# Kernel tuning notes

Hardware: AMD Instinct MI355X
Metric: run time of the kernel (lower is better)

Reference implementation:

```python
import jax, jax.numpy as jnp
import numpy as np

B_, L, HID = 2, 1024, 2048
N, H, P, NA = 128, 64, 64, 32   # state, heads, head_dim, rope angle pairs
DIN = 2 * H * P + 2 * N + 3 * H + NA  # 8672
EPS = 1e-5
A_FLOOR = 1e-4


def setup_inputs() -> dict:
    key = jax.random.key(0)
    k0, k1, k2 = jax.random.split(key, 3)
    hidden_states = jax.random.normal(k0, (B_, L, HID), jnp.float32)
    in_proj_w = jax.random.normal(k1, (DIN, HID), jnp.float32) * 0.02
    out_proj_w = jax.random.normal(k2, (HID, H * P), jnp.float32) * 0.02
    # dt_bias init exactly as in the torch module
    rng = np.random.default_rng(0)
    dt = np.exp(rng.random(H) * (np.log(0.1) - np.log(0.001)) + np.log(0.001))
    dt = np.clip(dt, 1e-4, None)
    dt_bias = jnp.asarray(dt + np.log(-np.expm1(-dt)), jnp.float32)
    return {
        'hidden_states': hidden_states,
        'in_proj_w': in_proj_w,
        'dt_bias': dt_bias,
        'B_bias': jnp.ones((H, N), jnp.float32),
        'C_bias': jnp.ones((H, N), jnp.float32),
        'B_norm_w': jnp.ones((N,), jnp.float32),
        'C_norm_w': jnp.ones((N,), jnp.float32),
        'D': jnp.ones((H,), jnp.float32),
        'out_proj_w': out_proj_w,
    }


def _rmsnorm(x, w):
    var = jnp.mean(jnp.square(x), axis=-1, keepdims=True)
    return x * jax.lax.rsqrt(var + EPS) * w


def _forward(hidden_states, in_proj_w, dt_bias, B_bias, C_bias,
             B_norm_w, C_norm_w, D, out_proj_w):
    b, l, _ = hidden_states.shape
    proj = hidden_states @ in_proj_w.T  # (b,l,DIN)
    splits = np.cumsum([H * P, H * P, N, N, H, H, H])
    z, x, Braw, Craw, dd_dt, dd_A, trap, angles = jnp.split(proj, splits, axis=-1)
    z = z.reshape(b, l, H, P)
    x = x.reshape(b, l, H, P)
    # data-dependent A (per token, per head), clamped
    A = jnp.minimum(-jax.nn.softplus(dd_A.astype(jnp.float32)), -A_FLOOR)
    DT = jax.nn.softplus(dd_dt + dt_bias)          # (b,l,H)
    decay = jnp.exp(A * DT)                        # (b,l,H)
    lam = jax.nn.sigmoid(trap)                     # trapezoidal weight (b,l,H)
    # RMSNorm then per-head input-independent bias (n_groups=1, mimo_rank=1)
    Bn = _rmsnorm(Braw, B_norm_w)[:, :, None, :] + B_bias  # (b,l,H,N)
    Cn = _rmsnorm(Craw, C_norm_w)[:, :, None, :] + C_bias  # (b,l,H,N)
    # blockwise rotary on first 2*NA state dims, cumulative data-dependent phase
    phase = jnp.cumsum(angles[:, :, None, :].astype(jnp.float32) * DT[..., None], axis=1)  # (b,l,H,NA)
    cos, sin = jnp.cos(phase), jnp.sin(phase)

    def rope(v):
        v1, v2, rest = v[..., :NA], v[..., NA:2 * NA], v[..., 2 * NA:]
        return jnp.concatenate([v1 * cos - v2 * sin, v1 * sin + v2 * cos, rest], axis=-1)

    Bh = rope(Bn.astype(jnp.float32))
    Ch = rope(Cn.astype(jnp.float32))
    u = (x * DT[..., None]).astype(jnp.float32)    # (b,l,H,P)

    # selective scan with generalized trapezoidal discretization:
    # h_t = a_t h_{t-1} + (1-lam_t) u_t B_t^T + lam_t a_t u_{t-1} B_{t-1}^T
    def step(carry, inp):
        h, Gp = carry
        Bt, Ct, ut, dec, lm = inp
        G = ut[..., :, None] * Bt[..., None, :]    # (b,H,P,N)
        h = dec[..., None, None] * h + (1.0 - lm)[..., None, None] * G \
            + (lm * dec)[..., None, None] * Gp
        y = jnp.einsum('bhpn,bhn->bhp', h, Ct)
        return (h, G), y

    h0 = jnp.zeros((b, H, P, N), jnp.float32)
    xs = (Bh.transpose(1, 0, 2, 3), Ch.transpose(1, 0, 2, 3),
          u.transpose(1, 0, 2, 3), decay.transpose(1, 0, 2), lam.transpose(1, 0, 2))
    _, ys = jax.lax.scan(step, (h0, h0), xs)       # (l,b,H,P)
    y = ys.transpose(1, 0, 2, 3)
    y = y + D[None, None, :, None] * x             # skip connection
    y = y * jax.nn.silu(z)                         # output gate (Z path in kernel)
    y = y.reshape(b, l, H * P)
    return y @ out_proj_w.T


def reference(hidden_states, in_proj_w, dt_bias, B_bias, C_bias,
              B_norm_w, C_norm_w, D, out_proj_w):
    return _forward(hidden_states, in_proj_w, dt_bias, B_bias, C_bias,
                    B_norm_w, C_norm_w, D, out_proj_w)
```

## Files before the change

kernel.cpp:

```cpp
#include <hip/hip_runtime.h>
#include <hip/hip_bf16.h>
#include <cstdint>
#include <cstddef>

#define DEVINL __device__ __forceinline__

typedef __attribute__((ext_vector_type(8))) short bf16x8;
typedef __attribute__((ext_vector_type(4))) float f32x4;

DEVINL float bf2f(unsigned short u){
  union { unsigned u32; float f; } cv; cv.u32 = ((unsigned)u) << 16; return cv.f;
}
DEVINL unsigned short f2bf(float f){
  union { float f; unsigned u32; } cv; cv.f = f;
  unsigned u = cv.u32;
  return (unsigned short)((u + 0x7FFFu + ((u >> 16) & 1u)) >> 16);
}
DEVINL float softplusf(float x){ return x > 20.f ? x : log1pf(expf(x)); }

DEVINL void g2l16(const void* gptr, void* ldsptr){
  __builtin_amdgcn_global_load_lds(
      (const __attribute__((address_space(1))) unsigned int*)gptr,
      (__attribute__((address_space(3))) unsigned int*)(uintptr_t)ldsptr,
      16, 0, 0);
}

DEVINL int swzb(int row, int col){ return row*256 + ((col*2) ^ ((row&7)<<4)); }
DEVINL void ldsw_write8(unsigned short* b, int row, int col, bf16x8 v){
  *(bf16x8*)((char*)b + swzb(row,col)) = v;
}
DEVINL bf16x8 ldsw_read8(const unsigned short* b, int row, int col){
  return *(const bf16x8*)((const char*)b + swzb(row,col));
}
DEVINL void ldsw_write1(unsigned short* b, int row, int col, unsigned short v){
  *(unsigned short*)((char*)b + swzb(row,col)) = v;
}
DEVINL unsigned short ldsw_read1(const unsigned short* b, int row, int col){
  return *(const unsigned short*)((const char*)b + swzb(row,col));
}

DEVINL unsigned long long pack4(float4 v){
  return (unsigned long long)f2bf(v.x)
       | ((unsigned long long)f2bf(v.y) << 16)
       | ((unsigned long long)f2bf(v.z) << 32)
       | ((unsigned long long)f2bf(v.w) << 48);
}

__global__ __launch_bounds__(256) void k_conv3(
    const float* __restrict__ a, unsigned short* __restrict__ oa, int nba,
    const float* __restrict__ b, unsigned short* __restrict__ ob, int nbb,
    const float* __restrict__ c, unsigned short* __restrict__ oc)
{
  const float* in; unsigned short* out; long blk;
  if ((int)blockIdx.x < nba)            { in = a; out = oa; blk = blockIdx.x; }
  else if ((int)blockIdx.x < nba + nbb) { in = b; out = ob; blk = blockIdx.x - nba; }
  else                                  { in = c; out = oc; blk = blockIdx.x - nba - nbb; }
  long i = (blk * 256 + threadIdx.x) * 8;
  float4 v0 = *(const float4*)(in + i);
  float4 v1 = *(const float4*)(in + i + 4);
  unsigned long long pk[2] = { pack4(v0), pack4(v1) };
  *(bf16x8*)(out + i) = *(const bf16x8*)pk;
}

template<bool OUT_BF16, int BN>
__global__ __launch_bounds__(256) void k_gemm_bt(
    const unsigned short* __restrict__ A,
    const unsigned short* __restrict__ Bt,
    void* __restrict__ Cout,
    int K, int Nrows, int Npad, int xm, int tmx, int tnx)
{
  constexpr int NB = BN / 32;
  __shared__ unsigned short Asub[128*64];
  __shared__ unsigned short Bsub[BN*64];
  const int tid = threadIdx.x;
  const int x = blockIdx.x & 7, i = blockIdx.x >> 3;
  const int rt = (x % xm) * tmx + (i % tmx);
  const int ct = (x / xm) * tnx + (i / tmx);
  const int lane = tid & 63, wave = tid >> 6;
  const int wr = wave >> 1, wc = wave & 1;
  const int fr = lane & 15;
  const int fq = lane >> 4;

  const int srow0 = tid >> 3;
  const int sgrp  = (tid & 7) ^ ((tid >> 3) & 7);
  size_t aoff[4], boff[NB];
  #pragma unroll
  for (int j = 0; j < 4; j++){
    int row = j*32 + srow0;
    aoff[j] = (size_t)(rt*128 + row) * K + sgrp*8;
  }
  #pragma unroll
  for (int j = 0; j < NB; j++){
    int row = j*32 + srow0;
    int brow = ct*BN + row; if (brow > Nrows-1) brow = Nrows-1;
    boff[j] = (size_t)brow * K + sgrp*8;
  }

  f32x4 acc[4][NB] = {};

  for (int k0 = 0; k0 < K; k0 += 64){
    #pragma unroll
    for (int j = 0; j < 4; j++)
      g2l16(A + aoff[j] + k0, (char*)Asub + (j*256 + tid)*16);
    #pragma unroll
    for (int j = 0; j < NB; j++)
      g2l16(Bt + boff[j] + k0, (char*)Bsub + (j*256 + tid)*16);
    asm volatile("s_waitcnt vmcnt(0)" ::: "memory");
    __syncthreads();

    #pragma unroll
    for (int kk = 0; kk < 2; kk++){
      bf16x8 af[4], bfr[NB];
      const int slot = (kk*4 + fq) ^ (fr & 7);
      #pragma unroll
      for (int j = 0; j < 4; j++){
        int ra = wr*64 + j*16 + fr;
        af[j] = *(const bf16x8*)((const char*)Asub + ra*128 + slot*16);
      }
      #pragma unroll
      for (int j = 0; j < NB; j++){
        int rb = wc*(BN/2) + j*16 + fr;
        bfr[j] = *(const bf16x8*)((const char*)Bsub + rb*128 + slot*16);
      }
      #pragma unroll
      for (int mi = 0; mi < 4; mi++)
        #pragma unroll
        for (int ni = 0; ni < NB; ni++)
          acc[mi][ni] = __builtin_amdgcn_mfma_f32_16x16x32_bf16(af[mi], bfr[ni], acc[mi][ni], 0, 0, 0);
    }
    __syncthreads();
  }

  const int er = (lane >> 4) * 4;
  const int ec = lane & 15;
  #pragma unroll
  for (int mi = 0; mi < 4; mi++){
    #pragma unroll
    for (int ni = 0; ni < NB; ni++){
      const int row = rt*128 + wr*64 + mi*16 + er;
      const int col = ct*BN + wc*(BN/2) + ni*16 + ec;
      #pragma unroll
      for (int r = 0; r < 4; r++){
        if (OUT_BF16)
          ((unsigned short*)Cout)[(size_t)(row+r)*Npad + col] = f2bf(acc[mi][ni][r]);
        else
          ((float*)Cout)[(size_t)(row+r)*Npad + col] = acc[mi][ni][r];
      }
    }
  }
}

__global__ __launch_bounds__(256) void k_gemm2sk(
    const unsigned short* __restrict__ A,
    const unsigned short* __restrict__ Bt,
    float* __restrict__ out, float* __restrict__ part)
{
  constexpr int K = 4096, BN = 64, NB = 2;
  __shared__ unsigned short Asub[128*64];
  __shared__ unsigned short Bsub[BN*64];
  const int tid = threadIdx.x;
  const int half = (int)(blockIdx.x >> 9);
  const int bid  = (int)(blockIdx.x & 511);
  const int kbeg = half * 2048;
  float* dst = half ? part : out;
  const int x = bid & 7, i = bid >> 3;
  const int rt = (x % 4) * 4 + (i % 4);
  const int ct = (x / 4) * 16 + (i / 4);
  const int lane = tid & 63, wave = tid >> 6;
  const int wr = wave >> 1, wc = wave & 1;
  const int fr = lane & 15;
  const int fq = lane >> 4;

  const int srow0 = tid >> 3;
  const int sgrp  = (tid & 7) ^ ((tid >> 3) & 7);
  size_t aoff[4], boff[NB];
  #pragma unroll
  for (int j = 0; j < 4; j++){
    int row = j*32 + srow0;
    aoff[j] = (size_t)(rt*128 + row) * K + sgrp*8;
  }
  #pragma unroll
  for (int j = 0; j < NB; j++){
    int row = j*32 + srow0;
    boff[j] = (size_t)(ct*BN + row) * K + sgrp*8;
  }

  f32x4 acc[4][NB] = {};

  for (int k0 = kbeg; k0 < kbeg + 2048; k0 += 64){
    #pragma unroll
    for (int j = 0; j < 4; j++)
      g2l16(A + aoff[j] + k0, (char*)Asub + (j*256 + tid)*16);
    #pragma unroll
    for (int j = 0; j < NB; j++)
      g2l16(Bt + boff[j] + k0, (char*)Bsub + (j*256 + tid)*16);
    asm volatile("s_waitcnt vmcnt(0)" ::: "memory");
    __syncthreads();

    #pragma unroll
    for (int kk = 0; kk < 2; kk++){
      bf16x8 af[4], bfr[NB];
      const int slot = (kk*4 + fq) ^ (fr & 7);
      #pragma unroll
      for (int j = 0; j < 4; j++){
        int ra = wr*64 + j*16 + fr;
        af[j] = *(const bf16x8*)((const char*)Asub + ra*128 + slot*16);
      }
      #pragma unroll
      for (int j = 0; j < NB; j++){
        int rb = wc*(BN/2) + j*16 + fr;
        bfr[j] = *(const bf16x8*)((const char*)Bsub + rb*128 + slot*16);
      }
      #pragma unroll
      for (int mi = 0; mi < 4; mi++)
        #pragma unroll
        for (int ni = 0; ni < NB; ni++)
          acc[mi][ni] = __builtin_amdgcn_mfma_f32_16x16x32_bf16(af[mi], bfr[ni], acc[mi][ni], 0, 0, 0);
    }
    __syncthreads();
  }

  const int er = (lane >> 4) * 4;
  const int ec = lane & 15;
  #pragma unroll
  for (int mi = 0; mi < 4; mi++){
    #pragma unroll
    for (int ni = 0; ni < NB; ni++){
      const int row = rt*128 + wr*64 + mi*16 + er;
      const int col = ct*BN + wc*(BN/2) + ni*16 + ec;
      #pragma unroll
      for (int r = 0; r < 4; r++)
        dst[(size_t)(row+r)*2048 + col] = acc[mi][ni][r];
    }
  }
}

__global__ __launch_bounds__(256) void k_addout(
    float* __restrict__ out, const float* __restrict__ part)
{
  long i = ((long)blockIdx.x*256 + threadIdx.x) * 4;
  float4 a = *(const float4*)(out + i);
  float4 b = *(const float4*)(part + i);
  a.x += b.x; a.y += b.y; a.z += b.z; a.w += b.w;
  *(float4*)(out + i) = a;
}

__global__ __launch_bounds__(512) void k_prep(
    const unsigned short* __restrict__ proj, const float* __restrict__ Bw,
    const float* __restrict__ Cw, const float* __restrict__ dtb,
    unsigned short* __restrict__ Bb2, unsigned short* __restrict__ Cb2,
    float* __restrict__ DTt, float* __restrict__ lamt,
    float* __restrict__ clcb, float* __restrict__ gb,
    unsigned short* __restrict__ cosb, unsigned short* __restrict__ sinb)
{
  const int tid = threadIdx.x;
  __shared__ float dtL[1024], lamL[1024];
  __shared__ float part[16][32];
  __shared__ float red[16];

  if (blockIdx.x >= 128){
    int row = (int)(blockIdx.x - 128)*4 + (tid >> 7);
    int n = tid & 127;
    size_t base = (size_t)row * 8704;
    float bv = bf2f(proj[base + 8192 + n]);
    float cv = bf2f(proj[base + 8320 + n]);
    float sb = bv*bv, sc = cv*cv;
    #pragma unroll
    for (int m = 1; m < 64; m <<= 1){ sb += __shfl_xor(sb, m, 64); sc += __shfl_xor(sc, m, 64); }
    int w = tid >> 6;
    if ((tid & 63) == 0){ red[w*2] = sb; red[w*2+1] = sc; }
    __syncthreads();
    int rw = (tid >> 7) * 2;
    sb = red[rw*2]   + red[rw*2+2];
    sc = red[rw*2+1] + red[rw*2+3];
    float rb = rsqrtf(sb*(1.f/128.f) + 1e-5f);
    float rc = rsqrtf(sc*(1.f/128.f) + 1e-5f);
    Bb2[row*128 + n] = f2bf(bv*rb*Bw[n]);
    Cb2[row*128 + n] = f2bf(cv*rc*Cw[n]);
    return;
  }

  const int bh = blockIdx.x, b = bh >> 6, h = bh & 63;
  const size_t sbase = (size_t)bh * 1024;
  const int lane = tid & 63;
  float ld0, ld1;
  {
    int l0 = tid*2;
    #pragma unroll
    for (int q = 0; q < 2; q++){
      int l = l0 + q;
      size_t pb = (size_t)(b*1024 + l) * 8704;
      float dd_dt = bf2f(proj[pb + 8448 + h]);
      float dd_A  = bf2f(proj[pb + 8512 + h]);
      float trap  = bf2f(proj[pb + 8576 + h]);
      float DT  = softplusf(dd_dt + dtb[h]);
      float A   = -fmaxf(softplusf(dd_A), 1e-4f);
      float lam = 1.f / (1.f + expf(-trap));
      dtL[l] = DT; lamL[l] = lam;
      if (q == 0) ld0 = A*DT; else ld1 = A*DT;
      DTt[sbase+l] = DT; lamt[sbase+l] = lam;
    }
  }
  __syncthreads();
  {
    float p1 = ld0 + ld1;
    float tot = p1;
    float incl = tot;
    #pragma unroll
    for (int off = 1; off < 64; off <<= 1){
      float u = __shfl_up(incl, off, 64);
      if (lane >= off) incl += u;
    }
    float excl = incl - tot;
    int l0 = tid*2;
    clcb[sbase+l0]   = excl + ld0;
    clcb[sbase+l0+1] = excl + p1;
    #pragma unroll
    for (int q = 0; q < 2; q++){
      int l = l0 + q;
      int ln = (l == 1023) ? 1023 : l + 1;
      gb[sbase+l] = 1.f - lamL[l] + lamL[ln];
    }
  }
  int na = tid & 31, c = tid >> 5;
  float s = 0.f;
  for (int q = 0; q < 64; q++){
    int l = c*64 + q; int row = b*1024 + l;
    float ang = bf2f(proj[(size_t)row*8704 + 8640 + na]);
    s = fmaf(ang, dtL[l], s);
  }
  part[c][na] = s;
  __syncthreads();
  float off = 0.f;
  for (int cc = 0; cc < c; cc++) off += part[cc][na];
  float ph = off;
  for (int q = 0; q < 64; q++){
    int l = c*64 + q; int row = b*1024 + l;
    float ang = bf2f(proj[(size_t)row*8704 + 8640 + na]);
    ph = fmaf(ang, dtL[l], ph);
    float sn, cs;
    __sincosf(ph, &sn, &cs);
    size_t o = ((size_t)row*64 + h)*32 + na;
    cosb[o] = f2bf(cs); sinb[o] = f2bf(sn);
  }
}

__global__ __launch_bounds__(512, 1) void k_intra(
    const unsigned short* __restrict__ proj,
    const unsigned short* __restrict__ Bb2, const unsigned short* __restrict__ Cb2,
    const float* __restrict__ Bbias, const float* __restrict__ Cbias,
    const unsigned short* __restrict__ cosb, const unsigned short* __restrict__ sinb,
    const float* __restrict__ DTt, const float* __restrict__ clcb,
    const float* __restrict__ gb, const float* __restrict__ lamt,
    const float* __restrict__ Dv, unsigned short* __restrict__ ybf,
    unsigned short* __restrict__ Gbuf)
{
  const int c = blockIdx.x & 7, bh = blockIdx.x >> 3;
  const int b = bh >> 6, h = bh & 63;
  const int tid = threadIdx.x, lane = tid & 63, wave = tid >> 6;
  const int wr = wave >> 2, wc = wave & 3;
  const int fr = lane & 15, fq = lane >> 4;

  __shared__ __align__(16) unsigned short Cs[128*128];
  __shared__ __align__(16) unsigned short Bs[128*128];
  __shared__ __align__(16) unsigned short BTs[128*128];
  __shared__ __align__(16) unsigned short Uts[64*128];
  __shared__ float clcs[128], lams[128], gs[128], wUs[128], dts[128];
  __shared__ float biasB[128], biasC[128];

  const int base = b*1024 + c*128;
  const size_t shbase = (size_t)bh * 1024;
  const float Dh = Dv[h];

  if (tid < 128){
    int l = c*128 + tid;
    clcs[tid] = clcb[shbase + l];
    dts[tid]  = DTt[shbase + l];
    lams[tid] = lamt[shbase + l];
    gs[tid]   = gb[shbase + l];
    biasB[tid] = Bbias[h*128 + tid];
  } else if (tid < 256){
    biasC[tid-128] = Cbias[h*128 + tid-128];
  }
  __syncthreads();
  if (tid < 128) wUs[tid] = __expf(clcs[127] - clcs[tid]) * gs[tid];

  {
    const int t = tid >> 2, q = tid & 3;
    const int grow = base + t;
    const size_t roff = (size_t)grow*128;
    if (q == 0){
      bf16x8 cc[4], sv[4];
      #pragma unroll
      for (int j = 0; j < 4; j++){
        cc[j] = *(const bf16x8*)(cosb + ((size_t)grow*64 + h)*32 + j*8);
        sv[j] = *(const bf16x8*)(sinb + ((size_t)grow*64 + h)*32 + j*8);
      }
      #pragma unroll
      for (int j = 0; j < 4; j++){
        bf16x8 vlo = *(const bf16x8*)(Cb2 + roff + j*8);
        bf16x8 vhi = *(const bf16x8*)(Cb2 + roff + 32 + j*8);
        bf16x8 olo, ohi;
        #pragma unroll
        for (int e = 0; e < 8; e++){
          float a = bf2f((unsigned short)vlo[e]) + biasC[j*8+e];
          float d = bf2f((unsigned short)vhi[e]) + biasC[32+j*8+e];
          float cf = bf2f((unsigned short)cc[j][e]);
          float sf = bf2f((unsigned short)sv[j][e]);
          olo[e] = (short)f2bf(a*cf - d*sf);
          ohi[e] = (short)f2bf(a*sf + d*cf);
        }
        ldsw_write8(Cs, t, j*8, olo);
        ldsw_write8(Cs, t, 32 + j*8, ohi);
      }
    } else if (q == 1){
      #pragma unroll
      for (int j = 0; j < 8; j++){
        bf16x8 v = *(const bf16x8*)(Cb2 + roff + 64 + j*8);
        bf16x8 o;
        #pragma unroll
        for (int e = 0; e < 8; e++) o[e] = (short)f2bf(bf2f((unsigned short)v[e]) + biasC[64+j*8+e]);
        ldsw_write8(Cs, t, 64 + j*8, o);
      }
    } else if (q == 2){
      bf16x8 cc[4], sv[4];
      #pragma unroll
      for (int j = 0; j < 4; j++){
        cc[j] = *(const bf16x8*)(cosb + ((size_t)grow*64 + h)*32 + j*8);
        sv[j] = *(const bf16x8*)(sinb + ((size_t)grow*64 + h)*32 + j*8);
      }
      #pragma unroll
      for (int j = 0; j < 4; j++){
        bf16x8 vlo = *(const bf16x8*)(Bb2 + roff + j*8);
        bf16x8 vhi = *(const bf16x8*)(Bb2 + roff + 32 + j*8);
        bf16x8 olo, ohi;
        #pragma unroll
        for (int e = 0; e < 8; e++){
          float a = bf2f((unsigned short)vlo[e]) + biasB[j*8+e];
          float d = bf2f((unsigned short)vhi[e]) + biasB[32+j*8+e];
          float cf = bf2f((unsigned short)cc[j][e]);
          float sf = bf2f((unsigned short)sv[j][e]);
          olo[e] = (short)f2bf(a*cf - d*sf);
          ohi[e] = (short)f2bf(a*sf + d*cf);
        }
        ldsw_write8(Bs, t, j*8, olo);
        ldsw_write8(Bs, t, 32 + j*8, ohi);
        #pragma unroll
        for (int e = 0; e < 8; e++){
          ldsw_write1(BTs, j*8+e, t, (unsigned short)olo[e]);
          ldsw_write1(BTs, 32+j*8+e, t, (unsigned short)ohi[e]);
        }
      }
    } else {
      #pragma unroll
      for (int j = 0; j < 8; j++){
        bf16x8 v = *(const bf16x8*)(Bb2 + roff + 64 + j*8);
        bf16x8 o;
        #pragma unroll
        for (int e = 0; e < 8; e++) o[e] = (short)f2bf(bf2f((unsigned short)v[e]) + biasB[64+j*8+e]);
        ldsw_write8(Bs, t, 64 + j*8, o);
        #pragma unroll
        for (int e = 0; e < 8; e++) ldsw_write1(BTs, 64+j*8+e, t, (unsigned short)o[e]);
      }
    }
  }
  {
    const int jr = tid >> 3;
    const int p0 = (tid & 7) * 8;
    #pragma unroll
    for (int q = 0; q < 2; q++){
      int j = q*64 + jr;
      size_t pb = (size_t)(base + j) * 8704;
      bf16x8 v = *(const bf16x8*)(proj + pb + 4096 + h*64 + p0);
      float dj = dts[j];
      #pragma unroll
      for (int e = 0; e < 8; e++)
        ldsw_write1(Uts, p0+e, j, f2bf(bf2f((unsigned short)v[e]) * dj));
    }
  }
  __syncthreads();

  f32x4 acc1[4][2];
  #pragma unroll
  for (int mi = 0; mi < 4; mi++)
    #pragma unroll
    for (int ni = 0; ni < 2; ni++)
      acc1[mi][ni] = (f32x4){0.f,0.f,0.f,0.f};
  #pragma unroll
  for (int ks = 0; ks < 4; ks++){
    bf16x8 af[4], bj[2];
    #pragma unroll
    for (int mi = 0; mi < 4; mi++) af[mi] = ldsw_read8(Cs, wr*64+mi*16+fr, ks*32+fq*8);
    #pragma unroll
    for (int ni = 0; ni < 2; ni++) bj[ni] = ldsw_read8(Bs, wc*32+ni*16+fr, ks*32+fq*8);
    #pragma unroll
    for (int mi = 0; mi < 4; mi++)
      #pragma unroll
      for (int ni = 0; ni < 2; ni++)
        acc1[mi][ni] = __builtin_amdgcn_mfma_f32_16x16x32_bf16(af[mi], bj[ni], acc1[mi][ni], 0,0,0);
  }
  unsigned short pr[4][2][4];
  int jj[2]; float clcj[2], gj[2];
  #pragma unroll
  for (int ni = 0; ni < 2; ni++){ jj[ni] = wc*32+ni*16+fr; clcj[ni] = clcs[jj[ni]]; gj[ni] = gs[jj[ni]]; }
  #pragma unroll
  for (int mi = 0; mi < 4; mi++){
    #pragma unroll
    for (int r = 0; r < 4; r++){
      int t = wr*64+mi*16+fq*4+r;
      float ct_ = clcs[t], lt = lams[t];
      #pragma unroll
      for (int ni = 0; ni < 2; ni++){
        int j = jj[ni];
        float w = (j < t) ? __expf(ct_ - clcj[ni])*gj[ni] : ((j == t) ? (1.f - lt) : 0.f);
        pr[mi][ni][r] = f2bf(acc1[mi][ni][r] * w);
      }
    }
  }
  __syncthreads();
  #pragma unroll
  for (int mi = 0; mi < 4; mi++)
    #pragma unroll
    for (int ni = 0; ni < 2; ni++)
      #pragma unroll
      for (int r = 0; r < 4; r++)
        ldsw_write1(Bs, wr*64+mi*16+fq*4+r, wc*32+ni*16+fr, pr[mi][ni][r]);
  __syncthreads();

  f32x4 acc2[4];
  #pragma unroll
  for (int mi = 0; mi < 4; mi++) acc2[mi] = (f32x4){0.f,0.f,0.f,0.f};
  #pragma unroll
  for (int ks = 0; ks < 4; ks++){
    bf16x8 af[4], uj;
    #pragma unroll
    for (int mi = 0; mi < 4; mi++) af[mi] = ldsw_read8(Bs, wr*64+mi*16+fr, ks*32+fq*8);
    uj = ldsw_read8(Uts, wc*16+fr, ks*32+fq*8);
    #pragma unroll
    for (int mi = 0; mi < 4; mi++)
      acc2[mi] = __builtin_amdgcn_mfma_f32_16x16x32_bf16(af[mi], uj, acc2[mi], 0,0,0);
  }
  f32x4 accS[2][2];
  #pragma unroll
  for (int mi = 0; mi < 2; mi++)
    #pragma unroll
    for (int ni = 0; ni < 2; ni++)
      accS[mi][ni] = (f32x4){0.f,0.f,0.f,0.f};
  #pragma unroll
  for (int ks = 0; ks < 4; ks++){
    bf16x8 au[2], bn[2];
    #pragma unroll
    for (int mi = 0; mi < 2; mi++){
      bf16x8 raw = ldsw_read8(Uts, wr*32+mi*16+fr, ks*32+fq*8);
      #pragma unroll
      for (int e = 0; e < 8; e++){
        float f = bf2f((unsigned short)raw[e]) * wUs[ks*32+fq*8+e];
        au[mi][e] = (short)f2bf(f);
      }
    }
    #pragma unroll
    for (int ni = 0; ni < 2; ni++) bn[ni] = ldsw_read8(BTs, wc*32+ni*16+fr, ks*32+fq*8);
    #pragma unroll
    for (int mi = 0; mi < 2; mi++)
      #pragma unroll
      for (int ni = 0; ni < 2; ni++)
        accS[mi][ni] = __builtin_amdgcn_mfma_f32_16x16x32_bf16(au[mi], bn[ni], accS[mi][ni], 0,0,0);
  }

  #pragma unroll
  for (int mi = 0; mi < 4; mi++){
    #pragma unroll
    for (int r = 0; r < 4; r++){
      int t = wr*64+mi*16+fq*4+r;
      int p = wc*16+fr;
      float xv = bf2f(ldsw_read1(Uts, p, t)) / fmaxf(dts[t], 1e-30f);
      float o = acc2[mi][r] + Dh*xv;
      ybf[(size_t)(base + t)*4096 + h*64 + p] = f2bf(o);
    }
  }
  #pragma unroll
  for (int mi = 0; mi < 2; mi++)
    #pragma unroll
    for (int ni = 0; ni < 2; ni++)
      #pragma unroll
      for (int r = 0; r < 4; r++){
        int p = wr*32+mi*16+fq*4+r;
        int n = wc*32+ni*16+fr;
        Gbuf[(size_t)blockIdx.x*8192 + p*128 + n] = f2bf(accS[mi][ni][r]);
      }
}

__global__ __launch_bounds__(256) void k_scanstate(
    const float* __restrict__ clcb, unsigned short* __restrict__ Gbuf)
{
  const int bh = blockIdx.x, tid = threadIdx.x;
  float S[32];
  #pragma unroll
  for (int q = 0; q < 32; q++) S[q] = 0.f;
  const size_t gbase = (size_t)bh*65536 + (size_t)tid*32;
  for (int c = 0; c < 8; c++){
    float decEnd = __expf(clcb[(size_t)bh*1024 + c*128 + 127]);
    unsigned short* p = Gbuf + gbase + (size_t)c*8192;
    bf16x8 g[4], s[4];
    #pragma unroll
    for (int q = 0; q < 4; q++) g[q] = *(const bf16x8*)(p + q*8);
    #pragma unroll
    for (int q = 0; q < 4; q++)
      #pragma unroll
      for (int e = 0; e < 8; e++) s[q][e] = (short)f2bf(S[q*8+e]);
    #pragma unroll
    for (int q = 0; q < 4; q++) *(bf16x8*)(p + q*8) = s[q];
    #pragma unroll
    for (int q = 0; q < 4; q++)
      #pragma unroll
      for (int e = 0; e < 8; e++)
        S[q*8+e] = decEnd*S[q*8+e] + bf2f((unsigned short)g[q][e]);
  }
}

__global__ __launch_bounds__(256) void k_inter(
    const unsigned short* __restrict__ proj,
    const unsigned short* __restrict__ Cb2, const float* __restrict__ Cbias,
    const unsigned short* __restrict__ cosb, const unsigned short* __restrict__ sinb,
    const float* __restrict__ clcb, const unsigned short* __restrict__ Sprev,
    unsigned short* __restrict__ ybf,
    const float* __restrict__ wo, unsigned short* __restrict__ wobf)
{
  if (blockIdx.x >= 1024){
    long i = (((long)blockIdx.x - 1024) * 256 + threadIdx.x) * 4;
    float4 v = *(const float4*)(wo + i);
    *(unsigned long long*)(wobf + i) = pack4(v);
    return;
  }
  const int c = blockIdx.x & 7, bh = blockIdx.x >> 3;
  const int b = bh >> 6, h = bh & 63;
  const int tid = threadIdx.x, lane = tid & 63, wave = tid >> 6;
  const int wr = wave >> 1, wc = wave & 1;
  const int fr = lane & 15, fq = lane >> 4;

  __shared__ __align__(16) unsigned short Cs[128*128];
  __shared__ __align__(16) unsigned short Ss[64*128];
  __shared__ float expclcs[128], biasC[128];

  const int base = b*1024 + c*128;

  if (tid < 128){
    expclcs[tid] = __expf(clcb[(size_t)bh*1024 + c*128 + tid]);
    biasC[tid] = Cbias[h*128 + tid];
  }
  __syncthreads();

  {
    const int t = tid >> 1, half = tid & 1;
    const int grow = base + t;
    const size_t roff = (size_t)grow*128 + half*64;
    if (half == 0){
      bf16x8 cc[4], sv[4];
      #pragma unroll
      for (int j = 0; j < 4; j++){
        cc[j] = *(const bf16x8*)(cosb + ((size_t)grow*64 + h)*32 + j*8);
        sv[j] = *(const bf16x8*)(sinb + ((size_t)grow*64 + h)*32 + j*8);
      }
      #pragma unroll
      for (int j = 0; j < 4; j++){
        bf16x8 vlo = *(const bf16x8*)(Cb2 + roff + j*8);
        bf16x8 vhi = *(const bf16x8*)(Cb2 + roff + 32 + j*8);
        bf16x8 olo, ohi;
        #pragma unroll
        for (int e = 0; e < 8; e++){
          float a = bf2f((unsigned short)vlo[e]) + biasC[j*8+e];
          float d = bf2f((unsigned short)vhi[e]) + biasC[32+j*8+e];
          float cf = bf2f((unsigned short)cc[j][e]);
          float sf = bf2f((unsigned short)sv[j][e]);
          olo[e] = (short)f2bf(a*cf - d*sf);
          ohi[e] = (short)f2bf(a*sf + d*cf);
        }
        ldsw_write8(Cs, t, j*8, olo);
        ldsw_write8(Cs, t, 32 + j*8, ohi);
      }
    } else {
      #pragma unroll
      for (int j = 0; j < 8; j++){
        bf16x8 v = *(const bf16x8*)(Cb2 + roff + j*8);
        bf16x8 o;
        #pragma unroll
        for (int e = 0; e < 8; e++) o[e] = (short)f2bf(bf2f((unsigned short)v[e]) + biasC[64+j*8+e]);
        ldsw_write8(Cs, t, 64 + j*8, o);
      }
    }
  }
  {
    const unsigned short* src = Sprev + (size_t)blockIdx.x*8192 + (size_t)tid*32;
    #pragma unroll
    for (int j = 0; j < 4; j++){
      bf16x8 v = *(const bf16x8*)(src + j*8);
      int f = tid*32 + j*8;
      ldsw_write8(Ss, f >> 7, f & 127, v);
    }
  }
  __syncthreads();

  f32x4 acc[4][2];
  #pragma unroll
  for (int mi = 0; mi < 4; mi++)
    #pragma unroll
    for (int ni = 0; ni < 2; ni++)
      acc[mi][ni] = (f32x4){0.f,0.f,0.f,0.f};
  #pragma unroll
  for (int ks = 0; ks < 4; ks++){
    bf16x8 af[4], sj[2];
    #pragma unroll
    for (int mi = 0; mi < 4; mi++) af[mi] = ldsw_read8(Cs, wr*64+mi*16+fr, ks*32+fq*8);
    #pragma unroll
    for (int ni = 0; ni < 2; ni++) sj[ni] = ldsw_read8(Ss, wc*32+ni*16+fr, ks*32+fq*8);
    #pragma unroll
    for (int mi = 0; mi < 4; mi++)
      #pragma unroll
      for (int ni = 0; ni < 2; ni++)
        acc[mi][ni] = __builtin_amdgcn_mfma_f32_16x16x32_bf16(af[mi], sj[ni], acc[mi][ni], 0,0,0);
  }

  #pragma unroll
  for (int mi = 0; mi < 4; mi++){
    #pragma unroll
    for (int ni = 0; ni < 2; ni++){
      #pragma unroll
      for (int r = 0; r < 4; r++){
        int t = wr*64+mi*16+fq*4+r;
        int p = wc*32+ni*16+fr;
        size_t yoff = (size_t)(base + t)*4096 + h*64 + p;
        float y = bf2f(ybf[yoff]) + expclcs[t]*acc[mi][ni][r];
        float zv = bf2f(proj[(size_t)(base + t)*8704 + h*64 + p]);
        float sl = zv / (1.f + __expf(-zv));
        ybf[yoff] = f2bf(y * sl);
      }
    }
  }
}

extern "C" void kernel_launch(void* const* d_in, const int* in_sizes, int n_in,
                              void* d_out, int out_size, void* d_ws, size_t ws_size,
                              hipStream_t stream)
{
  const float* hs    = (const float*)d_in[0];
  const float* w1    = (const float*)d_in[1];
  const float* dtb   = (const float*)d_in[2];
  const float* Bbias = (const float*)d_in[3];
  const float* Cbias = (const float*)d_in[4];
  const float* Bw    = (const float*)d_in[5];
  const float* Cw    = (const float*)d_in[6];
  const float* Dv    = (const float*)d_in[7];
  const float* wo    = (const float*)d_in[8];
  float* out = (float*)d_out;
  char* ws = (char*)d_ws;

  unsigned short* projbf = (unsigned short*)(ws + 0UL);
  float* gemm2part       = (float*)(ws + 0UL);
  unsigned short* W1bf   = (unsigned short*)(ws + 35651584UL);
  unsigned short* Gbuf   = W1bf;
  unsigned short* ybf    = (unsigned short*)(ws + 52428800UL);
  unsigned short* hsbf   = (unsigned short*)(ws + 71172096UL);
  unsigned short* cosb   = hsbf;
  unsigned short* sinb   = (unsigned short*)(ws + 79560704UL);
  float* DTt    = (float*)(ws + 87949312UL);
  float* lamt   = (float*)(ws + 88997888UL);
  float* clcb   = (float*)(ws + 89522176UL);
  float* gb     = (float*)(ws + 90046464UL);
  unsigned short* Bb2 = (unsigned short*)(ws + 90570752UL);
  unsigned short* Cb2 = (unsigned short*)(ws + 91095040UL);
  if (ws_size < 91619328UL) return;

  const bool bigws = (ws_size >= 91619328UL + 16777216UL);
  unsigned short* Wobf = bigws ? (unsigned short*)(ws + 91619328UL) : W1bf;

  (void)in_sizes; (void)n_in; (void)out_size;

  k_conv3<<<bigws ? 14816 : 10720, 256, 0, stream>>>(
      w1, W1bf, 8672, hs, hsbf, 2048, wo, Wobf);
  k_gemm_bt<true, 128><<<1088, 256, 0, stream>>>(hsbf, W1bf, projbf, 2048, 8672, 8704, 2, 8, 17);
  k_prep<<<640, 512, 0, stream>>>(projbf, Bw, Cw, dtb, Bb2, Cb2,
                                  DTt, lamt, clcb, gb, cosb, sinb);
  k_intra<<<1024, 512, 0, stream>>>(projbf, Bb2, Cb2, Bbias, Cbias,
                                    cosb, sinb, DTt, clcb, gb, lamt, Dv, ybf, Gbuf);
  k_scanstate<<<128, 256, 0, stream>>>(clcb, Gbuf);
  k_inter<<<bigws ? 1024 : 9216, 256, 0, stream>>>(
      projbf, Cb2, Cbias, cosb, sinb, clcb, Gbuf, ybf, wo, Wobf);
  k_gemm2sk<<<1024, 256, 0, stream>>>(ybf, Wobf, out, gemm2part);
  k_addout<<<4096, 256, 0, stream>>>(out, gemm2part);
}
```

Measured before the change: 298.5 us.

## Fuse inter-chunk state scan into k_inter and drop k_scanstate kernel

Removes the separate k_scanstate launch. Each k_inter block now rebuilds its starting state by walking the per-chunk state contributions of all earlier chunks, keeping the sum in fp32 registers. This avoids one kernel launch and the serial 128-block pass that read and wrote Gbuf, at the price of redundant work: chunk c rereads c earlier chunk buffers. k_intra also computes and stores its chunk state earlier in the kernel, which may change register pressure and overlap.

```diff
diff --git a/kernel.cpp b/kernel.cpp
--- a/kernel.cpp
+++ b/kernel.cpp
@@ -499,6 +499,42 @@
       for (int ni = 0; ni < 2; ni++)
         acc1[mi][ni] = __builtin_amdgcn_mfma_f32_16x16x32_bf16(af[mi], bj[ni], acc1[mi][ni], 0,0,0);
   }
+  f32x4 accS[2][2];
+  #pragma unroll
+  for (int mi = 0; mi < 2; mi++)
+    #pragma unroll
+    for (int ni = 0; ni < 2; ni++)
+      accS[mi][ni] = (f32x4){0.f,0.f,0.f,0.f};
+  #pragma unroll
+  for (int ks = 0; ks < 4; ks++){
+    bf16x8 au[2], bn[2];
+    #pragma unroll
+    for (int mi = 0; mi < 2; mi++){
+      bf16x8 raw = ldsw_read8(Uts, wr*32+mi*16+fr, ks*32+fq*8);
+      #pragma unroll
+      for (int e = 0; e < 8; e++){
+        float f = bf2f((unsigned short)raw[e]) * wUs[ks*32+fq*8+e];
+        au[mi][e] = (short)f2bf(f);
+      }
+    }
+    #pragma unroll
+    for (int ni = 0; ni < 2; ni++) bn[ni] = ldsw_read8(BTs, wc*32+ni*16+fr, ks*32+fq*8);
+    #pragma unroll
+    for (int mi = 0; mi < 2; mi++)
+      #pragma unroll
+      for (int ni = 0; ni < 2; ni++)
+        accS[mi][ni] = __builtin_amdgcn_mfma_f32_16x16x32_bf16(au[mi], bn[ni], accS[mi][ni], 0,0,0);
+  }
+  #pragma unroll
+  for (int mi = 0; mi < 2; mi++)
+    #pragma unroll
+    for (int ni = 0; ni < 2; ni++)
+      #pragma unroll
+      for (int r = 0; r < 4; r++){
+        int p = wr*32+mi*16+fq*4+r;
+        int n = wc*32+ni*16+fr;
+        Gbuf[(size_t)blockIdx.x*8192 + p*128 + n] = f2bf(accS[mi][ni][r]);
+      }
   unsigned short pr[4][2][4];
   int jj[2]; float clcj[2], gj[2];
   #pragma unroll
@@ -539,32 +575,6 @@
     #pragma unroll
     for (int mi = 0; mi < 4; mi++)
       acc2[mi] = __builtin_amdgcn_mfma_f32_16x16x32_bf16(af[mi], uj, acc2[mi], 0,0,0);
-  }
-  f32x4 accS[2][2];
-  #pragma unroll
-  for (int mi = 0; mi < 2; mi++)
-    #pragma unroll
-    for (int ni = 0; ni < 2; ni++)
-      accS[mi][ni] = (f32x4){0.f,0.f,0.f,0.f};
-  #pragma unroll
-  for (int ks = 0; ks < 4; ks++){
-    bf16x8 au[2], bn[2];
-    #pragma unroll
-    for (int mi = 0; mi < 2; mi++){
-      bf16x8 raw = ldsw_read8(Uts, wr*32+mi*16+fr, ks*32+fq*8);
-      #pragma unroll
-      for (int e = 0; e < 8; e++){
-        float f = bf2f((unsigned short)raw[e]) * wUs[ks*32+fq*8+e];
-        au[mi][e] = (short)f2bf(f);
-      }
-    }
-    #pragma unroll
-    for (int ni = 0; ni < 2; ni++) bn[ni] = ldsw_read8(BTs, wc*32+ni*16+fr, ks*32+fq*8);
-    #pragma unroll
-    for (int mi = 0; mi < 2; mi++)
-      #pragma unroll
-      for (int ni = 0; ni < 2; ni++)
-        accS[mi][ni] = __builtin_amdgcn_mfma_f32_16x16x32_bf16(au[mi], bn[ni], accS[mi][ni], 0,0,0);
   }
 
   #pragma unroll
@@ -578,51 +588,13 @@
       ybf[(size_t)(base + t)*4096 + h*64 + p] = f2bf(o);
     }
   }
-  #pragma unroll
-  for (int mi = 0; mi < 2; mi++)
-    #pragma unroll
-    for (int ni = 0; ni < 2; ni++)
-      #pragma unroll
-      for (int r = 0; r < 4; r++){
-        int p = wr*32+mi*16+fq*4+r;
-        int n = wc*32+ni*16+fr;
-        Gbuf[(size_t)blockIdx.x*8192 + p*128 + n] = f2bf(accS[mi][ni][r]);
-      }
-}
-
-__global__ __launch_bounds__(256) void k_scanstate(
-    const float* __restrict__ clcb, unsigned short* __restrict__ Gbuf)
-{
-  const int bh = blockIdx.x, tid = threadIdx.x;
-  float S[32];
-  #pragma unroll
-  for (int q = 0; q < 32; q++) S[q] = 0.f;
-  const size_t gbase = (size_t)bh*65536 + (size_t)tid*32;
-  for (int c = 0; c < 8; c++){
-    float decEnd = __expf(clcb[(size_t)bh*1024 + c*128 + 127]);
-    unsigned short* p = Gbuf + gbase + (size_t)c*8192;
-    bf16x8 g[4], s[4];
-    #pragma unroll
-    for (int q = 0; q < 4; q++) g[q] = *(const bf16x8*)(p + q*8);
-    #pragma unroll
-    for (int q = 0; q < 4; q++)
-      #pragma unroll
-      for (int e = 0; e < 8; e++) s[q][e] = (short)f2bf(S[q*8+e]);
-    #pragma unroll
-    for (int q = 0; q < 4; q++) *(bf16x8*)(p + q*8) = s[q];
-    #pragma unroll
-    for (int q = 0; q < 4; q++)
-      #pragma unroll
-      for (int e = 0; e < 8; e++)
-        S[q*8+e] = decEnd*S[q*8+e] + bf2f((unsigned short)g[q][e]);
-  }
 }
 
 __global__ __launch_bounds__(256) void k_inter(
     const unsigned short* __restrict__ proj,
     const unsigned short* __restrict__ Cb2, const float* __restrict__ Cbias,
     const unsigned short* __restrict__ cosb, const unsigned short* __restrict__ sinb,
-    const float* __restrict__ clcb, const unsigned short* __restrict__ Sprev,
+    const float* __restrict__ clcb, const unsigned short* __restrict__ Gbuf,
     unsigned short* __restrict__ ybf,
     const float* __restrict__ wo, unsigned short* __restrict__ wobf)
 {
@@ -650,6 +622,30 @@
   }
   __syncthreads();
 
+  {
+    float S[32];
+    #pragma unroll
+    for (int q = 0; q < 32; q++) S[q] = 0.f;
+    for (int cc = 0; cc < c; cc++){
+      float decEnd = __expf(clcb[(size_t)bh*1024 + cc*128 + 127]);
+      const unsigned short* p = Gbuf + (size_t)(bh*8 + cc)*8192 + (size_t)tid*32;
+      #pragma unroll
+      for (int q = 0; q < 4; q++){
+        bf16x8 g = *(const bf16x8*)(p + q*8);
+        #pragma unroll
+        for (int e = 0; e < 8; e++)
+          S[q*8+e] = decEnd*S[q*8+e] + bf2f((unsigned short)g[e]);
+      }
+    }
+    #pragma unroll
+    for (int q = 0; q < 4; q++){
+      bf16x8 v;
+      #pragma unroll
+      for (int e = 0; e < 8; e++) v[e] = (short)f2bf(S[q*8+e]);
+      int f = tid*32 + q*8;
+      ldsw_write8(Ss, f >> 7, f & 127, v);
+    }
+  }
   {
     const int t = tid >> 1, half = tid & 1;
     const int grow = base + t;
@@ -687,15 +683,6 @@
         for (int e = 0; e < 8; e++) o[e] = (short)f2bf(bf2f((unsigned short)v[e]) + biasC[64+j*8+e]);
         ldsw_write8(Cs, t, 64 + j*8, o);
       }
-    }
-  }
-  {
-    const unsigned short* src = Sprev + (size_t)blockIdx.x*8192 + (size_t)tid*32;
-    #pragma unroll
-    for (int j = 0; j < 4; j++){
-      bf16x8 v = *(const bf16x8*)(src + j*8);
-      int f = tid*32 + j*8;
-      ldsw_write8(Ss, f >> 7, f & 127, v);
     }
   }
   __syncthreads();
@@ -782,7 +769,6 @@
                                   DTt, lamt, clcb, gb, cosb, sinb);
   k_intra<<<1024, 512, 0, stream>>>(projbf, Bb2, Cb2, Bbias, Cbias,
                                     cosb, sinb, DTt, clcb, gb, lamt, Dv, ybf, Gbuf);
-  k_scanstate<<<128, 256, 0, stream>>>(clcb, Gbuf);
   k_inter<<<bigws ? 1024 : 9216, 256, 0, stream>>>(
       projbf, Cb2, Cbias, cosb, sinb, clcb, Gbuf, ybf, wo, Wobf);
   k_gemm2sk<<<1024, 256, 0, stream>>>(ybf, Wobf, out, gemm2part);
```

After: 298.5 us. No clear change (-0.0%).
